# Kernel optimization log

Measured on AMD Instinct MI355X. Metric: run time of the kernel, lower is better.

Reference implementation:

```python
import jax, jax.numpy as jnp
import numpy as np

DIM = 256      # model dim E
H = 8          # num_heads
M = 32         # ball_size
TOPK = 2       # selected balls per query
N = 256        # number of balls
NM = N * M     # total points (8192)


def setup_inputs() -> dict:
    key = jax.random.key(0)
    k1, k2 = jax.random.split(key)
    x = jax.random.normal(k1, (NM, DIM), dtype=jnp.float32)
    pos = jax.random.normal(k2, (NM, 3), dtype=jnp.float32)
    return {"x": x, "pos": pos}


def reference(x, pos):
    e = DIM // H                      # per-head dim
    scale = DIM ** (-0.5)             # note: module scales by full dim, not head dim
    # pe_proj(compute_rel_pos(pos)) == 0 in the source (dead code), so x is unchanged.
    # qkv repeat + decompose '(H E K)' makes q == k == v == x reshaped per head.
    xh = x.reshape(N, M, H, e).transpose(0, 2, 1, 3)   # (n, H, m, e)
    q = xh
    k = xh
    v = xh

    # --- select_balls (runs under torch.no_grad) ---
    qf = jax.lax.stop_gradient(q).transpose(1, 0, 2, 3).reshape(H, NM, e)   # (H, nm, e)
    kmean = jax.lax.stop_gradient(k).mean(axis=2).transpose(1, 0, 2)        # (H, n, e)
    sim = jax.nn.softmax(jnp.einsum('hqe,hne->hqn', qf, kmean) * scale, axis=-1)
    topv, topi = jax.lax.top_k(sim, TOPK)               # (H, nm, topk)

    # straight-through gates (values were computed under no_grad -> constant 1.0)
    gates = topv + jax.lax.stop_gradient(1.0 - topv)
    # mask: each topk slot repeated over the m leaves of its ball
    fmask = jnp.repeat(topv > 1e-10, M, axis=-1)        # (H, nm, topk*m)

    # --- gather selected balls (avoid the torch repeat-then-gather blowup) ---
    kh = k.transpose(1, 0, 2, 3)                        # (H, n, m, e)
    vh = v.transpose(1, 0, 2, 3)
    gather = jax.vmap(lambda t, i: t[i])                # per-head fancy gather
    ksel = gather(kh, topi)                             # (H, nm, topk, m, e)
    vsel = gather(vh, topi)
    ksel = gates[..., None, None] * ksel                # use_diff_topk=True
    ksel = ksel.reshape(H, NM, TOPK * M, e)
    vsel = vsel.reshape(H, NM, TOPK * M, e)

    # --- masked attention over gathered keys ---
    qq = q.transpose(1, 0, 2, 3).reshape(H, NM, e)      # (H, nm, e)
    fsim = jnp.einsum('hqe,hqse->hqs', qq, ksel) * scale
    fsim = jnp.where(fmask, fsim, -jnp.finfo(fsim.dtype).max)
    attn = jax.nn.softmax(fsim, axis=-1)
    out = jnp.einsum('hqs,hqse->hqe', attn, vsel)       # (H, nm, e)
    return out.transpose(1, 0, 2).reshape(NM, DIM)      # (nm, H*e)
```

## Files before the change

### kernel.cpp

```cpp
#include <hip/hip_runtime.h>

#define FLT_BIG 3.402823466e38f

static __device__ __forceinline__ bool better(float v1, int i1, float v2, int i2) {
  return (v1 > v2) || ((v1 == v2) && (i1 < i2));
}

__global__ void kmeanT_kernel(const float* __restrict__ x, float* __restrict__ kmT) {
  const int n = blockIdx.x;
  const int t = threadIdx.x;
  const float* base = x + n * 32 * 256 + t;
  float acc = 0.f;
  #pragma unroll
  for (int j = 0; j < 32; ++j) acc += base[j * 256];
  const int h = t >> 5, e = t & 31;
  kmT[h * 8192 + e * 256 + n] = acc * (1.0f / 32.0f);
}

__global__ __launch_bounds__(256) void select_kernel(const float* __restrict__ x,
                                                     const float* __restrict__ kmT,
                                                     int2* __restrict__ sel) {
  __shared__ float smem[32 * 260];
  const int h = blockIdx.x >> 8;
  const int qg = blockIdx.x & 255;
  const int t = threadIdx.x;
  const int w = t >> 6, lane = t & 63;

  {
    const int r = t >> 3, c = t & 7;
    *(float4*)&smem[r * 32 + c * 4] =
        *(const float4*)(x + (qg * 32 + r) * 256 + h * 32 + c * 4);
  }
  __syncthreads();

  const float4* kmp = (const float4*)(kmT + h * 8192);
  float acc[8][4];
  #pragma unroll
  for (int qq = 0; qq < 8; ++qq)
    #pragma unroll
    for (int j = 0; j < 4; ++j) acc[qq][j] = 0.f;

  float4 ka[4], kb[4];
  #pragma unroll
  for (int d = 0; d < 4; ++d) ka[d] = kmp[d * 64 + lane];

  #pragma unroll
  for (int e0 = 0; e0 < 8; ++e0) {
    float4* cur = (e0 & 1) ? kb : ka;
    float4* nxt = (e0 & 1) ? ka : kb;
    if (e0 < 7) {
      #pragma unroll
      for (int d = 0; d < 4; ++d) nxt[d] = kmp[((e0 + 1) * 4 + d) * 64 + lane];
    }
    #pragma unroll
    for (int qq = 0; qq < 8; ++qq) {
      const float4 qf = *(const float4*)&smem[(w * 8 + qq) * 32 + e0 * 4];
      acc[qq][0] = fmaf(qf.w, cur[3].x, fmaf(qf.z, cur[2].x, fmaf(qf.y, cur[1].x, fmaf(qf.x, cur[0].x, acc[qq][0]))));
      acc[qq][1] = fmaf(qf.w, cur[3].y, fmaf(qf.z, cur[2].y, fmaf(qf.y, cur[1].y, fmaf(qf.x, cur[0].y, acc[qq][1]))));
      acc[qq][2] = fmaf(qf.w, cur[3].z, fmaf(qf.z, cur[2].z, fmaf(qf.y, cur[1].z, fmaf(qf.x, cur[0].z, acc[qq][2]))));
      acc[qq][3] = fmaf(qf.w, cur[3].w, fmaf(qf.z, cur[2].w, fmaf(qf.y, cur[1].w, fmaf(qf.x, cur[0].w, acc[qq][3]))));
    }
  }
  __syncthreads();

  #pragma unroll
  for (int qq = 0; qq < 8; ++qq) {
    *(float4*)&smem[(w * 8 + qq) * 260 + lane * 4] =
        make_float4(acc[qq][0], acc[qq][1], acc[qq][2], acc[qq][3]);
  }
  __syncthreads();

  const int qloc = t >> 3, ch = t & 7;
  const float* rowp = &smem[qloc * 260 + ch * 32];
  float a1 = -FLT_BIG, a2 = -FLT_BIG;
  int j1 = 0, j2 = 0;
  #pragma unroll
  for (int i = 0; i < 8; ++i) {
    const float4 v4 = *(const float4*)(rowp + i * 4);
    const int b0 = ch * 32 + i * 4;
    if (v4.x > a1) { a2 = a1; j2 = j1; a1 = v4.x; j1 = b0; }
    else if (v4.x > a2) { a2 = v4.x; j2 = b0; }
    if (v4.y > a1) { a2 = a1; j2 = j1; a1 = v4.y; j1 = b0 + 1; }
    else if (v4.y > a2) { a2 = v4.y; j2 = b0 + 1; }
    if (v4.z > a1) { a2 = a1; j2 = j1; a1 = v4.z; j1 = b0 + 2; }
    else if (v4.z > a2) { a2 = v4.z; j2 = b0 + 2; }
    if (v4.w > a1) { a2 = a1; j2 = j1; a1 = v4.w; j1 = b0 + 3; }
    else if (v4.w > a2) { a2 = v4.w; j2 = b0 + 3; }
  }

  int pk = j1 | (j2 << 16);
  #pragma unroll
  for (int m = 1; m <= 4; m <<= 1) {
    const float b1 = __shfl_xor(a1, m);
    const float b2 = __shfl_xor(a2, m);
    const int bpk = __shfl_xor(pk, m);
    const int bj1 = bpk & 65535, bj2 = bpk >> 16;
    int c1 = pk & 65535, c2 = pk >> 16;
    if (better(b1, bj1, a1, c1)) {
      if (better(a1, c1, b2, bj2)) { a2 = a1; c2 = c1; } else { a2 = b2; c2 = bj2; }
      a1 = b1; c1 = bj1;
    } else if (better(b1, bj1, a2, c2)) { a2 = b1; c2 = bj1; }
    pk = c1 | (c2 << 16);
  }

  if (ch == 0) {
    sel[h * 8192 + qg * 32 + qloc] = make_int2(pk & 65535, pk >> 16);
  }
}

__global__ __launch_bounds__(256) void attn_kernel(const float* __restrict__ x,
                                                   const int2* __restrict__ sel,
                                                   float* __restrict__ out) {
  const int lane = threadIdx.x & 63;
  const int widx = threadIdx.x >> 6;
  const int task = blockIdx.x * 4 + widx;
  const int h = task >> 13;
  const int q = task & 8191;
  const int o = lane & 7;
  const int ro = lane >> 3;

  const int2 sv = sel[task];
  const int bA = sv.x, bB = sv.y;

  const float4 qf = *(const float4*)(x + q * 256 + h * 32 + o * 4);

  float4 kA[4], kB[4];
  const float* xa = x + bA * 8192 + ro * 256 + h * 32 + o * 4;
  const float* xb = x + bB * 8192 + ro * 256 + h * 32 + o * 4;
  #pragma unroll
  for (int i = 0; i < 4; ++i) {
    kA[i] = *(const float4*)(xa + i * 2048);
    kB[i] = *(const float4*)(xb + i * 2048);
  }

  float dA[4], dB[4];
  #pragma unroll
  for (int i = 0; i < 4; ++i) {
    float a = qf.x * kA[i].x; a = fmaf(qf.y, kA[i].y, a);
    a = fmaf(qf.z, kA[i].z, a); a = fmaf(qf.w, kA[i].w, a);
    dA[i] = a;
    float b = qf.x * kB[i].x; b = fmaf(qf.y, kB[i].y, b);
    b = fmaf(qf.z, kB[i].z, b); b = fmaf(qf.w, kB[i].w, b);
    dB[i] = b;
  }
  #pragma unroll
  for (int m = 1; m <= 4; m <<= 1) {
    #pragma unroll
    for (int i = 0; i < 4; ++i) {
      dA[i] += __shfl_xor(dA[i], m);
      dB[i] += __shfl_xor(dB[i], m);
    }
  }

  float pA[4], pB[4], psum = 0.f;
  #pragma unroll
  for (int i = 0; i < 4; ++i) {
    pA[i] = __expf(dA[i] * 0.0625f);
    pB[i] = __expf(dB[i] * 0.0625f);
    psum += pA[i] + pB[i];
  }
  #pragma unroll
  for (int m = 8; m <= 32; m <<= 1) psum += __shfl_xor(psum, m);

  float ox = 0.f, oy = 0.f, oz = 0.f, ow = 0.f;
  #pragma unroll
  for (int i = 0; i < 4; ++i) {
    ox = fmaf(pA[i], kA[i].x, ox); oy = fmaf(pA[i], kA[i].y, oy);
    oz = fmaf(pA[i], kA[i].z, oz); ow = fmaf(pA[i], kA[i].w, ow);
    ox = fmaf(pB[i], kB[i].x, ox); oy = fmaf(pB[i], kB[i].y, oy);
    oz = fmaf(pB[i], kB[i].z, oz); ow = fmaf(pB[i], kB[i].w, ow);
  }
  #pragma unroll
  for (int m = 8; m <= 32; m <<= 1) {
    ox += __shfl_xor(ox, m);
    oy += __shfl_xor(oy, m);
    oz += __shfl_xor(oz, m);
    ow += __shfl_xor(ow, m);
  }

  const float inv = 1.0f / psum;
  if (ro == 0) {
    *(float4*)(out + q * 256 + h * 32 + o * 4) =
        make_float4(ox * inv, oy * inv, oz * inv, ow * inv);
  }
}

extern "C" void kernel_launch(void* const* d_in, const int* in_sizes, int n_in,
                              void* d_out, int out_size, void* d_ws, size_t ws_size,
                              hipStream_t stream) {
  const float* x = (const float*)d_in[0];
  float* kmT = (float*)d_ws;
  int2* sel = (int2*)((char*)d_ws + 262144);
  float* out = (float*)d_out;

  kmeanT_kernel<<<256, 256, 0, stream>>>(x, kmT);
  select_kernel<<<2048, 256, 0, stream>>>(x, kmT, sel);
  attn_kernel<<<16384, 256, 0, stream>>>(x, sel, out);
}
```

Measured before the change: 60.11 us.

## Regroup attention by selected ball with atomic scatter lists and partial-sum combine

The select kernel now appends each (query, slot) pair to a per-(head, ball) list using atomic counters. A new ball-centric kernel stages one ball's 32 keys in shared memory and computes unnormalized softmax partials for every query that selected that ball. A combine kernel then adds the two partials per query and normalizes. This is meant to reuse each ball's keys from shared memory instead of gathering them per query. In exchange it adds a memset, atomics, a large partial buffer round-trip, load imbalance across balls and a 1024-entry cap per list that silently drops overflow. The new path only runs when the workspace is large enough.

```diff
diff --git a/kernel.cpp b/kernel.cpp
--- a/kernel.cpp
+++ b/kernel.cpp
@@ -19,7 +19,10 @@
 
 __global__ __launch_bounds__(256) void select_kernel(const float* __restrict__ x,
                                                      const float* __restrict__ kmT,
-                                                     int2* __restrict__ sel) {
+                                                     int2* __restrict__ sel,
+                                                     int* __restrict__ cnt,
+                                                     int* __restrict__ list,
+                                                     const int doScatter) {
   __shared__ float smem[32 * 260];
   const int h = blockIdx.x >> 8;
   const int qg = blockIdx.x & 255;
@@ -104,8 +107,117 @@
   }
 
   if (ch == 0) {
-    sel[h * 8192 + qg * 32 + qloc] = make_int2(pk & 65535, pk >> 16);
-  }
+    const int task = h * 8192 + qg * 32 + qloc;
+    const int b1 = pk & 65535, b2 = pk >> 16;
+    sel[task] = make_int2(b1, b2);
+    if (doScatter) {
+      const int c1i = h * 256 + b1;
+      const int p1 = atomicAdd(&cnt[c1i], 1);
+      if (p1 < 1024) list[c1i * 1024 + p1] = task * 2;
+      const int c2i = h * 256 + b2;
+      const int p2 = atomicAdd(&cnt[c2i], 1);
+      if (p2 < 1024) list[c2i * 1024 + p2] = task * 2 + 1;
+    }
+  }
+}
+
+__global__ __launch_bounds__(256) void ball_attn_kernel(const float* __restrict__ x,
+                                                        const int* __restrict__ cnt,
+                                                        const int* __restrict__ list,
+                                                        float* __restrict__ part) {
+  __shared__ float kt[32 * 32];
+  const int cell = blockIdx.x;
+  const int n = min(cnt[cell], 1024);
+  if (n == 0) return;
+  const int h = cell >> 8, ball = cell & 255;
+  const int t = threadIdx.x;
+  const int w = t >> 6, lane = t & 63;
+
+  {
+    const int j = t >> 3, c = t & 7;
+    *(float4*)&kt[j * 32 + c * 4] =
+        *(const float4*)(x + (ball * 32 + j) * 256 + h * 32 + c * 4);
+  }
+  __syncthreads();
+
+  for (int base = w * 64; base < n; base += 256) {
+    const int ei = base + lane;
+    const bool valid = ei < n;
+    const int ent = list[cell * 1024 + (valid ? ei : n - 1)];
+    const int q = (ent >> 1) & 8191;
+
+    float qv[32];
+    {
+      const float4* qp = (const float4*)(x + q * 256 + h * 32);
+      #pragma unroll
+      for (int c = 0; c < 8; ++c) {
+        const float4 f = qp[c];
+        qv[4 * c + 0] = f.x; qv[4 * c + 1] = f.y;
+        qv[4 * c + 2] = f.z; qv[4 * c + 3] = f.w;
+      }
+    }
+
+    float d[32];
+    #pragma unroll
+    for (int j = 0; j < 32; ++j) {
+      const float4* kr = (const float4*)&kt[j * 32];
+      float a = 0.f;
+      #pragma unroll
+      for (int c = 0; c < 8; ++c) {
+        const float4 kv = kr[c];
+        a = fmaf(qv[4 * c + 0], kv.x, a);
+        a = fmaf(qv[4 * c + 1], kv.y, a);
+        a = fmaf(qv[4 * c + 2], kv.z, a);
+        a = fmaf(qv[4 * c + 3], kv.w, a);
+      }
+      d[j] = a;
+    }
+
+    float psum = 0.f;
+    #pragma unroll
+    for (int j = 0; j < 32; ++j) {
+      d[j] = __expf(d[j] * 0.0625f);
+      psum += d[j];
+    }
+
+    float acc[32];
+    #pragma unroll
+    for (int e = 0; e < 32; ++e) acc[e] = 0.f;
+    #pragma unroll
+    for (int j = 0; j < 32; ++j) {
+      const float4* kr = (const float4*)&kt[j * 32];
+      const float pj = d[j];
+      #pragma unroll
+      for (int c = 0; c < 8; ++c) {
+        const float4 kv = kr[c];
+        acc[4 * c + 0] = fmaf(pj, kv.x, acc[4 * c + 0]);
+        acc[4 * c + 1] = fmaf(pj, kv.y, acc[4 * c + 1]);
+        acc[4 * c + 2] = fmaf(pj, kv.z, acc[4 * c + 2]);
+        acc[4 * c + 3] = fmaf(pj, kv.w, acc[4 * c + 3]);
+      }
+    }
+
+    if (valid) {
+      float* pr = part + (size_t)ent * 36;
+      pr[0] = psum;
+      #pragma unroll
+      for (int c = 0; c < 8; ++c)
+        *(float4*)(pr + 4 + c * 4) =
+            make_float4(acc[4 * c], acc[4 * c + 1], acc[4 * c + 2], acc[4 * c + 3]);
+    }
+  }
+}
+
+__global__ __launch_bounds__(256) void combine_kernel(const float* __restrict__ part,
+                                                      float* __restrict__ out) {
+  const int idx = blockIdx.x * 256 + threadIdx.x;
+  const int task = idx >> 5, e = idx & 31;
+  const float* p0 = part + (size_t)(task * 2) * 36;
+  const float* p1 = p0 + 36;
+  const float ps = p0[0] + p1[0];
+  const float v = (p0[4 + e] + p1[4 + e]) / ps;
+  const int h = task >> 13, q = task & 8191;
+  out[q * 256 + h * 32 + e] = v;
 }
 
 __global__ __launch_bounds__(256) void attn_kernel(const float* __restrict__ x,
@@ -121,7 +233,6 @@
 
   const int2 sv = sel[task];
   const int bA = sv.x, bB = sv.y;
-
   const float4 qf = *(const float4*)(x + q * 256 + h * 32 + o * 4);
 
   float4 kA[4], kB[4];
@@ -177,7 +288,6 @@
     oz += __shfl_xor(oz, m);
     ow += __shfl_xor(ow, m);
   }
-
   const float inv = 1.0f / psum;
   if (ro == 0) {
     *(float4*)(out + q * 256 + h * 32 + o * 4) =
@@ -189,11 +299,24 @@
                               void* d_out, int out_size, void* d_ws, size_t ws_size,
                               hipStream_t stream) {
   const float* x = (const float*)d_in[0];
-  float* kmT = (float*)d_ws;
-  int2* sel = (int2*)((char*)d_ws + 262144);
+  char* ws = (char*)d_ws;
+  float* kmT = (float*)ws;
+  int2* sel  = (int2*)(ws + 262144);
+  int* cnt   = (int*)(ws + 786432);
+  int* list  = (int*)(ws + 794624);
+  float* part = (float*)(ws + 9183232);
   float* out = (float*)d_out;
 
+  const bool big = ws_size >= (size_t)28057600;
+
   kmeanT_kernel<<<256, 256, 0, stream>>>(x, kmT);
-  select_kernel<<<2048, 256, 0, stream>>>(x, kmT, sel);
-  attn_kernel<<<16384, 256, 0, stream>>>(x, sel, out);
-}
+  if (big) {
+    hipMemsetAsync(cnt, 0, 2048 * sizeof(int), stream);
+    select_kernel<<<2048, 256, 0, stream>>>(x, kmT, sel, cnt, list, 1);
+    ball_attn_kernel<<<2048, 256, 0, stream>>>(x, cnt, list, part);
+    combine_kernel<<<8192, 256, 0, stream>>>(part, out);
+  } else {
+    select_kernel<<<2048, 256, 0, stream>>>(x, kmT, sel, cnt, list, 0);
+    attn_kernel<<<16384, 256, 0, stream>>>(x, sel, out);
+  }
+}
```

After: 196.6 us. 3.27x slower.

## Fuse ball selection and gathered attention into one kernel per query tile

Applied to the files above, without the earlier changes.

Merges the select and attention kernels into one kernel. Each block computes the query-to-ball-mean scores, does top-2 selection entirely in registers with a full-wave shuffle reduction instead of a shared-memory transpose, keeps the selections in shared memory, and then runs attention for its 32 queries with each wave looping over 8 queries. This removes one kernel launch, the global round-trip for the selection indices, and the re-read of the query rows. The cost is fewer blocks doing serialized per-query attention, which reduces the parallelism available to hide the latency of the gather loads.

```diff
diff --git a/kernel.cpp b/kernel.cpp
--- a/kernel.cpp
+++ b/kernel.cpp
@@ -17,10 +17,11 @@
   kmT[h * 8192 + e * 256 + n] = acc * (1.0f / 32.0f);
 }
 
-__global__ __launch_bounds__(256) void select_kernel(const float* __restrict__ x,
-                                                     const float* __restrict__ kmT,
-                                                     int2* __restrict__ sel) {
-  __shared__ float smem[32 * 260];
+__global__ __launch_bounds__(256) void fused_kernel(const float* __restrict__ x,
+                                                    const float* __restrict__ kmT,
+                                                    float* __restrict__ out) {
+  __shared__ float qtile[32 * 32];
+  __shared__ int2 selbuf[32];
   const int h = blockIdx.x >> 8;
   const int qg = blockIdx.x & 255;
   const int t = threadIdx.x;
@@ -28,7 +29,7 @@
 
   {
     const int r = t >> 3, c = t & 7;
-    *(float4*)&smem[r * 32 + c * 4] =
+    *(float4*)&qtile[r * 32 + c * 4] =
         *(const float4*)(x + (qg * 32 + r) * 256 + h * 32 + c * 4);
   }
   __syncthreads();
@@ -40,148 +41,127 @@
     #pragma unroll
     for (int j = 0; j < 4; ++j) acc[qq][j] = 0.f;
 
-  float4 ka[4], kb[4];
-  #pragma unroll
-  for (int d = 0; d < 4; ++d) ka[d] = kmp[d * 64 + lane];
+  {
+    float4 ka[4], kb[4];
+    #pragma unroll
+    for (int d = 0; d < 4; ++d) ka[d] = kmp[d * 64 + lane];
 
-  #pragma unroll
-  for (int e0 = 0; e0 < 8; ++e0) {
-    float4* cur = (e0 & 1) ? kb : ka;
-    float4* nxt = (e0 & 1) ? ka : kb;
-    if (e0 < 7) {
+    #pragma unroll
+    for (int e0 = 0; e0 < 8; ++e0) {
+      float4* cur = (e0 & 1) ? kb : ka;
+      float4* nxt = (e0 & 1) ? ka : kb;
+      if (e0 < 7) {
+        #pragma unroll
+        for (int d = 0; d < 4; ++d) nxt[d] = kmp[((e0 + 1) * 4 + d) * 64 + lane];
+      }
       #pragma unroll
-      for (int d = 0; d < 4; ++d) nxt[d] = kmp[((e0 + 1) * 4 + d) * 64 + lane];
-    }
-    #pragma unroll
-    for (int qq = 0; qq < 8; ++qq) {
-      const float4 qf = *(const float4*)&smem[(w * 8 + qq) * 32 + e0 * 4];
-      acc[qq][0] = fmaf(qf.w, cur[3].x, fmaf(qf.z, cur[2].x, fmaf(qf.y, cur[1].x, fmaf(qf.x, cur[0].x, acc[qq][0]))));
-      acc[qq][1] = fmaf(qf.w, cur[3].y, fmaf(qf.z, cur[2].y, fmaf(qf.y, cur[1].y, fmaf(qf.x, cur[0].y, acc[qq][1]))));
-      acc[qq][2] = fmaf(qf.w, cur[3].z, fmaf(qf.z, cur[2].z, fmaf(qf.y, cur[1].z, fmaf(qf.x, cur[0].z, acc[qq][2]))));
-      acc[qq][3] = fmaf(qf.w, cur[3].w, fmaf(qf.z, cur[2].w, fmaf(qf.y, cur[1].w, fmaf(qf.x, cur[0].w, acc[qq][3]))));
+      for (int qq = 0; qq < 8; ++qq) {
+        const float4 qf = *(const float4*)&qtile[(w * 8 + qq) * 32 + e0 * 4];
+        acc[qq][0] = fmaf(qf.w, cur[3].x, fmaf(qf.z, cur[2].x, fmaf(qf.y, cur[1].x, fmaf(qf.x, cur[0].x, acc[qq][0]))));
+        acc[qq][1] = fmaf(qf.w, cur[3].y, fmaf(qf.z, cur[2].y, fmaf(qf.y, cur[1].y, fmaf(qf.x, cur[0].y, acc[qq][1]))));
+        acc[qq][2] = fmaf(qf.w, cur[3].z, fmaf(qf.z, cur[2].z, fmaf(qf.y, cur[1].z, fmaf(qf.x, cur[0].z, acc[qq][2]))));
+        acc[qq][3] = fmaf(qf.w, cur[3].w, fmaf(qf.z, cur[2].w, fmaf(qf.y, cur[1].w, fmaf(qf.x, cur[0].w, acc[qq][3]))));
+      }
     }
   }
-  __syncthreads();
 
   #pragma unroll
   for (int qq = 0; qq < 8; ++qq) {
-    *(float4*)&smem[(w * 8 + qq) * 260 + lane * 4] =
-        make_float4(acc[qq][0], acc[qq][1], acc[qq][2], acc[qq][3]);
-  }
-  __syncthreads();
+    float a1 = acc[qq][0]; int c1i = 4 * lane;
+    float a2 = -FLT_BIG; int c2i = 0;
+    if (acc[qq][1] > a1) { a2 = a1; c2i = c1i; a1 = acc[qq][1]; c1i = 4 * lane + 1; }
+    else if (acc[qq][1] > a2) { a2 = acc[qq][1]; c2i = 4 * lane + 1; }
+    if (acc[qq][2] > a1) { a2 = a1; c2i = c1i; a1 = acc[qq][2]; c1i = 4 * lane + 2; }
+    else if (acc[qq][2] > a2) { a2 = acc[qq][2]; c2i = 4 * lane + 2; }
+    if (acc[qq][3] > a1) { a2 = a1; c2i = c1i; a1 = acc[qq][3]; c1i = 4 * lane + 3; }
+    else if (acc[qq][3] > a2) { a2 = acc[qq][3]; c2i = 4 * lane + 3; }
 
-  const int qloc = t >> 3, ch = t & 7;
-  const float* rowp = &smem[qloc * 260 + ch * 32];
-  float a1 = -FLT_BIG, a2 = -FLT_BIG;
-  int j1 = 0, j2 = 0;
-  #pragma unroll
-  for (int i = 0; i < 8; ++i) {
-    const float4 v4 = *(const float4*)(rowp + i * 4);
-    const int b0 = ch * 32 + i * 4;
-    if (v4.x > a1) { a2 = a1; j2 = j1; a1 = v4.x; j1 = b0; }
-    else if (v4.x > a2) { a2 = v4.x; j2 = b0; }
-    if (v4.y > a1) { a2 = a1; j2 = j1; a1 = v4.y; j1 = b0 + 1; }
-    else if (v4.y > a2) { a2 = v4.y; j2 = b0 + 1; }
-    if (v4.z > a1) { a2 = a1; j2 = j1; a1 = v4.z; j1 = b0 + 2; }
-    else if (v4.z > a2) { a2 = v4.z; j2 = b0 + 2; }
-    if (v4.w > a1) { a2 = a1; j2 = j1; a1 = v4.w; j1 = b0 + 3; }
-    else if (v4.w > a2) { a2 = v4.w; j2 = b0 + 3; }
+    int pk = c1i | (c2i << 16);
+    #pragma unroll
+    for (int m = 1; m <= 32; m <<= 1) {
+      const float b1 = __shfl_xor(a1, m);
+      const float b2 = __shfl_xor(a2, m);
+      const int bpk = __shfl_xor(pk, m);
+      const int bj1 = bpk & 65535, bj2 = bpk >> 16;
+      int c1 = pk & 65535, c2 = pk >> 16;
+      if (better(b1, bj1, a1, c1)) {
+        if (better(a1, c1, b2, bj2)) { a2 = a1; c2 = c1; } else { a2 = b2; c2 = bj2; }
+        a1 = b1; c1 = bj1;
+      } else if (better(b1, bj1, a2, c2)) { a2 = b1; c2 = bj1; }
+      pk = c1 | (c2 << 16);
+    }
+    if (lane == 0) selbuf[w * 8 + qq] = make_int2(pk & 65535, pk >> 16);
+    __builtin_amdgcn_sched_barrier(0);
   }
 
-  int pk = j1 | (j2 << 16);
-  #pragma unroll
-  for (int m = 1; m <= 4; m <<= 1) {
-    const float b1 = __shfl_xor(a1, m);
-    const float b2 = __shfl_xor(a2, m);
-    const int bpk = __shfl_xor(pk, m);
-    const int bj1 = bpk & 65535, bj2 = bpk >> 16;
-    int c1 = pk & 65535, c2 = pk >> 16;
-    if (better(b1, bj1, a1, c1)) {
-      if (better(a1, c1, b2, bj2)) { a2 = a1; c2 = c1; } else { a2 = b2; c2 = bj2; }
-      a1 = b1; c1 = bj1;
-    } else if (better(b1, bj1, a2, c2)) { a2 = b1; c2 = bj1; }
-    pk = c1 | (c2 << 16);
-  }
-
-  if (ch == 0) {
-    sel[h * 8192 + qg * 32 + qloc] = make_int2(pk & 65535, pk >> 16);
-  }
-}
-
-__global__ __launch_bounds__(256) void attn_kernel(const float* __restrict__ x,
-                                                   const int2* __restrict__ sel,
-                                                   float* __restrict__ out) {
-  const int lane = threadIdx.x & 63;
-  const int widx = threadIdx.x >> 6;
-  const int task = blockIdx.x * 4 + widx;
-  const int h = task >> 13;
-  const int q = task & 8191;
   const int o = lane & 7;
   const int ro = lane >> 3;
+  #pragma unroll 1
+  for (int qq = 0; qq < 8; ++qq) {
+    const int qloc = w * 8 + qq;
+    const int2 sv = selbuf[qloc];
+    const int bA = sv.x, bB = sv.y;
+    const float4 qf = *(const float4*)&qtile[qloc * 32 + o * 4];
 
-  const int2 sv = sel[task];
-  const int bA = sv.x, bB = sv.y;
-
-  const float4 qf = *(const float4*)(x + q * 256 + h * 32 + o * 4);
-
-  float4 kA[4], kB[4];
-  const float* xa = x + bA * 8192 + ro * 256 + h * 32 + o * 4;
-  const float* xb = x + bB * 8192 + ro * 256 + h * 32 + o * 4;
-  #pragma unroll
-  for (int i = 0; i < 4; ++i) {
-    kA[i] = *(const float4*)(xa + i * 2048);
-    kB[i] = *(const float4*)(xb + i * 2048);
-  }
-
-  float dA[4], dB[4];
-  #pragma unroll
-  for (int i = 0; i < 4; ++i) {
-    float a = qf.x * kA[i].x; a = fmaf(qf.y, kA[i].y, a);
-    a = fmaf(qf.z, kA[i].z, a); a = fmaf(qf.w, kA[i].w, a);
-    dA[i] = a;
-    float b = qf.x * kB[i].x; b = fmaf(qf.y, kB[i].y, b);
-    b = fmaf(qf.z, kB[i].z, b); b = fmaf(qf.w, kB[i].w, b);
-    dB[i] = b;
-  }
-  #pragma unroll
-  for (int m = 1; m <= 4; m <<= 1) {
+    float4 kA[4], kB[4];
+    const float* xa = x + bA * 8192 + ro * 256 + h * 32 + o * 4;
+    const float* xb = x + bB * 8192 + ro * 256 + h * 32 + o * 4;
     #pragma unroll
     for (int i = 0; i < 4; ++i) {
-      dA[i] += __shfl_xor(dA[i], m);
-      dB[i] += __shfl_xor(dB[i], m);
+      kA[i] = *(const float4*)(xa + i * 2048);
+      kB[i] = *(const float4*)(xb + i * 2048);
     }
-  }
 
-  float pA[4], pB[4], psum = 0.f;
-  #pragma unroll
-  for (int i = 0; i < 4; ++i) {
-    pA[i] = __expf(dA[i] * 0.0625f);
-    pB[i] = __expf(dB[i] * 0.0625f);
-    psum += pA[i] + pB[i];
-  }
-  #pragma unroll
-  for (int m = 8; m <= 32; m <<= 1) psum += __shfl_xor(psum, m);
+    float dA[4], dB[4];
+    #pragma unroll
+    for (int i = 0; i < 4; ++i) {
+      float a = qf.x * kA[i].x; a = fmaf(qf.y, kA[i].y, a);
+      a = fmaf(qf.z, kA[i].z, a); a = fmaf(qf.w, kA[i].w, a);
+      dA[i] = a;
+      float b = qf.x * kB[i].x; b = fmaf(qf.y, kB[i].y, b);
+      b = fmaf(qf.z, kB[i].z, b); b = fmaf(qf.w, kB[i].w, b);
+      dB[i] = b;
+    }
+    #pragma unroll
+    for (int m = 1; m <= 4; m <<= 1) {
+      #pragma unroll
+      for (int i = 0; i < 4; ++i) {
+        dA[i] += __shfl_xor(dA[i], m);
+        dB[i] += __shfl_xor(dB[i], m);
+      }
+    }
 
-  float ox = 0.f, oy = 0.f, oz = 0.f, ow = 0.f;
-  #pragma unroll
-  for (int i = 0; i < 4; ++i) {
-    ox = fmaf(pA[i], kA[i].x, ox); oy = fmaf(pA[i], kA[i].y, oy);
-    oz = fmaf(pA[i], kA[i].z, oz); ow = fmaf(pA[i], kA[i].w, ow);
-    ox = fmaf(pB[i], kB[i].x, ox); oy = fmaf(pB[i], kB[i].y, oy);
-    oz = fmaf(pB[i], kB[i].z, oz); ow = fmaf(pB[i], kB[i].w, ow);
-  }
-  #pragma unroll
-  for (int m = 8; m <= 32; m <<= 1) {
-    ox += __shfl_xor(ox, m);
-    oy += __shfl_xor(oy, m);
-    oz += __shfl_xor(oz, m);
-    ow += __shfl_xor(ow, m);
-  }
+    float pA[4], pB[4], psum = 0.f;
+    #pragma unroll
+    for (int i = 0; i < 4; ++i) {
+      pA[i] = __expf(dA[i] * 0.0625f);
+      pB[i] = __expf(dB[i] * 0.0625f);
+      psum += pA[i] + pB[i];
+    }
+    #pragma unroll
+    for (int m = 8; m <= 32; m <<= 1) psum += __shfl_xor(psum, m);
 
-  const float inv = 1.0f / psum;
-  if (ro == 0) {
-    *(float4*)(out + q * 256 + h * 32 + o * 4) =
-        make_float4(ox * inv, oy * inv, oz * inv, ow * inv);
+    float ox = 0.f, oy = 0.f, oz = 0.f, ow = 0.f;
+    #pragma unroll
+    for (int i = 0; i < 4; ++i) {
+      ox = fmaf(pA[i], kA[i].x, ox); oy = fmaf(pA[i], kA[i].y, oy);
+      oz = fmaf(pA[i], kA[i].z, oz); ow = fmaf(pA[i], kA[i].w, ow);
+      ox = fmaf(pB[i], kB[i].x, ox); oy = fmaf(pB[i], kB[i].y, oy);
+      oz = fmaf(pB[i], kB[i].z, oz); ow = fmaf(pB[i], kB[i].w, ow);
+    }
+    #pragma unroll
+    for (int m = 8; m <= 32; m <<= 1) {
+      ox += __shfl_xor(ox, m);
+      oy += __shfl_xor(oy, m);
+      oz += __shfl_xor(oz, m);
+      ow += __shfl_xor(ow, m);
+    }
+
+    const float inv = 1.0f / psum;
+    if (ro == 0) {
+      *(float4*)(out + (qg * 32 + qloc) * 256 + h * 32 + o * 4) =
+          make_float4(ox * inv, oy * inv, oz * inv, ow * inv);
+    }
   }
 }
 
@@ -190,10 +170,8 @@
                               hipStream_t stream) {
   const float* x = (const float*)d_in[0];
   float* kmT = (float*)d_ws;
-  int2* sel = (int2*)((char*)d_ws + 262144);
   float* out = (float*)d_out;
 
   kmeanT_kernel<<<256, 256, 0, stream>>>(x, kmT);
-  select_kernel<<<2048, 256, 0, stream>>>(x, kmT, sel);
-  attn_kernel<<<16384, 256, 0, stream>>>(x, sel, out);
+  fused_kernel<<<2048, 256, 0, stream>>>(x, kmT, out);
 }
```

After: 159.6 us. 2.66x slower.
